# Performance work log

Hardware: AMD Instinct MI355X
Metric: run time of the kernel (lower is better)

The kernel has to match this reference:

```python
import jax, jax.numpy as jnp
from jax import lax
import numpy as np

D_MODEL = 512
D_PROJ = 256
PATCH = 4
NL = 8
D_STATE = 16
D_CONV = 4
EXPAND = 2
D_INNER = EXPAND * D_MODEL          # 1024
DT_RANK = (D_MODEL + 15) // 16      # 32
B = 4
SEQ = 1024
NF = 1
EPS = 1e-5


def setup_inputs() -> dict:
    key = jax.random.key(0)
    ks = jax.random.split(key, 12)
    s = 0.02
    def rn(k, shape):
        return jax.random.normal(k, shape, jnp.float32) * s
    A_init = jnp.log(jnp.arange(1, D_STATE + 1, dtype=jnp.float32))  # (n,)
    return {
        "time_series": jax.random.normal(ks[0], (B, SEQ, NF), jnp.float32),
        "mask": jnp.ones((B, SEQ), jnp.int32),
        "emb_w": rn(ks[1], (D_MODEL, PATCH)),
        "emb_b": jnp.zeros((D_MODEL,), jnp.float32),
        "norm_w": jnp.ones((NL, D_MODEL), jnp.float32),
        "in_w": rn(ks[2], (NL, 2, 2 * D_INNER, D_MODEL)),
        "conv_w": rn(ks[3], (NL, 2, D_INNER, D_CONV)),
        "conv_b": jnp.zeros((NL, 2, D_INNER), jnp.float32),
        "xproj_w": rn(ks[4], (NL, 2, DT_RANK + 2 * D_STATE, D_INNER)),
        "dt_w": rn(ks[5], (NL, 2, D_INNER, DT_RANK)),
        "dt_b": jnp.full((NL, 2, D_INNER), float(np.log(np.expm1(0.01))), jnp.float32),
        "A_log": jnp.broadcast_to(A_init, (NL, 2, D_INNER, D_STATE)) + jnp.zeros((NL, 2, D_INNER, D_STATE), jnp.float32),
        "Dp": jnp.ones((NL, 2, D_INNER), jnp.float32),
        "out_w": rn(ks[6], (NL, 2, D_MODEL, D_INNER)),
        "proj_w": rn(ks[7], (PATCH * D_PROJ, D_MODEL)),
        "proj_b": jnp.zeros((PATCH * D_PROJ,), jnp.float32),
    }


def rmsnorm(x, w):
    return x * lax.rsqrt(jnp.mean(x * x, axis=-1, keepdims=True) + EPS) * w


def mamba(x, in_w, conv_w, conv_b, xproj_w, dt_w, dt_b, A_log, Dp, out_w):
    # x: (B, L, D_MODEL)
    Bsz, L, _ = x.shape
    xz = jnp.einsum('bld,ed->ble', x, in_w)                 # (B,L,2*d_inner)
    u, z = jnp.split(xz, 2, axis=-1)                         # each (B,L,d_inner)
    # depthwise causal conv1d along L
    u_t = jnp.transpose(u, (0, 2, 1))                        # (B,d_inner,L)
    u_pad = jnp.pad(u_t, ((0, 0), (0, 0), (D_CONV - 1, 0)))
    conv = lax.conv_general_dilated(
        u_pad, conv_w[:, None, :], window_strides=(1,), padding='VALID',
        feature_group_count=D_INNER, dimension_numbers=('NCH', 'OIH', 'NCH'))
    u = jax.nn.silu(jnp.transpose(conv + conv_b[None, :, None], (0, 2, 1)))  # (B,L,d_inner)
    x_dbl = jnp.einsum('ble,re->blr', u, xproj_w)            # (B,L,dt_rank+2n)
    dt, Bm, C = jnp.split(x_dbl, [DT_RANK, DT_RANK + D_STATE], axis=-1)
    delta = jax.nn.softplus(jnp.einsum('blr,er->ble', dt, dt_w) + dt_b)  # (B,L,d_inner)
    A = -jnp.exp(A_log)                                      # (d_inner,n)

    def step(h, inp):
        d_t, B_t, C_t, u_t = inp                             # (B,e),(B,n),(B,n),(B,e)
        dA = jnp.exp(d_t[..., None] * A)                     # (B,e,n)
        h = dA * h + (d_t * u_t)[..., None] * B_t[:, None, :]
        y = jnp.einsum('ben,bn->be', h, C_t)
        return h, y

    h0 = jnp.zeros((Bsz, D_INNER, D_STATE), x.dtype)
    xs = (jnp.moveaxis(delta, 1, 0), jnp.moveaxis(Bm, 1, 0),
          jnp.moveaxis(C, 1, 0), jnp.moveaxis(u, 1, 0))
    _, ys = lax.scan(step, h0, xs)                           # ys: (L,B,e)
    y = jnp.moveaxis(ys, 0, 1) + u * Dp
    y = y * jax.nn.silu(z)
    return jnp.einsum('ble,de->bld', y, out_w)               # (B,L,D_MODEL)


def reference(time_series, mask, emb_w, emb_b, norm_w, in_w, conv_w, conv_b,
              xproj_w, dt_w, dt_b, A_log, Dp, out_w, proj_w, proj_b):
    Bsz, S, F_ = time_series.shape
    NP = S // PATCH  # S is a multiple of PATCH
    patches = time_series.reshape(Bsz, NP, PATCH, F_)
    patches = jnp.transpose(patches, (0, 3, 1, 2)).reshape(Bsz, F_ * NP, PATCH)
    x = patches @ emb_w.T + emb_b                            # (B, F*NP, D_MODEL)
    for i in range(NL):
        res = x
        xn = rmsnorm(x, norm_w[i])
        yf = mamba(xn, in_w[i, 0], conv_w[i, 0], conv_b[i, 0], xproj_w[i, 0],
                   dt_w[i, 0], dt_b[i, 0], A_log[i, 0], Dp[i, 0], out_w[i, 0])
        yb = mamba(jnp.flip(xn, axis=1), in_w[i, 1], conv_w[i, 1], conv_b[i, 1],
                   xproj_w[i, 1], dt_w[i, 1], dt_b[i, 1], A_log[i, 1], Dp[i, 1], out_w[i, 1])
        x = yf + jnp.flip(yb, axis=1) + res
    proj = x @ proj_w.T + proj_b                             # (B, F*NP, PATCH*D_PROJ)
    le = proj.reshape(Bsz, F_, NP, PATCH, D_PROJ)
    le = jnp.transpose(le, (0, 2, 3, 1, 4)).reshape(Bsz, NP * PATCH, F_, D_PROJ)
    return le[:, :S]
```

## Files before the change

### kernel.cpp

```cpp
#include <hip/hip_runtime.h>
#include <hip/hip_bf16.h>

#define DM 512
#define DI 1024
#define DSTATE 16
#define DTR 32
#define NLAYER 8
#define BS 4
#define LL 256
#define MT 1024
#define DPROJ 256
#define CL 32
#define NCH (LL/CL)

typedef unsigned short u16;
typedef unsigned int u32;
typedef __attribute__((ext_vector_type(8))) short short8;
typedef __attribute__((ext_vector_type(4))) float f32x4;

__device__ __forceinline__ float sigmoidf_(float x){ return 1.f/(1.f+__expf(-x)); }

__device__ __forceinline__ u16 f2bf(float f){
  unsigned u = __float_as_uint(f);
  u = (u + 0x7FFF + ((u>>16)&1)) >> 16;
  return (u16)u;
}
__device__ __forceinline__ float bf2f(u16 v){
  return __uint_as_float(((unsigned)v) << 16);
}

template<int CTRL>
__device__ __forceinline__ float dpp_ror_add(float x){
  int y = __builtin_amdgcn_update_dpp(0, __float_as_int(x), CTRL, 0xF, 0xF, false);
  return x + __int_as_float(y);
}
__device__ __forceinline__ float sum16_dpp(float x){
  x = dpp_ror_add<0x128>(x);
  x = dpp_ror_add<0x124>(x);
  x = dpp_ror_add<0x122>(x);
  x = dpp_ror_add<0x121>(x);
  return x;
}

__global__ __launch_bounds__(256) void embed_k(const float* __restrict__ ts,
    const float* __restrict__ ew, const float* __restrict__ eb, float* __restrict__ x){
  int idx = blockIdx.x*256 + threadIdx.x;
  int m = idx >> 9, d = idx & 511;
  int b = m >> 8, np_ = m & 255;
  const float* t0 = ts + b*1024 + np_*4;
  float acc = eb[d];
  #pragma unroll
  for (int p=0;p<4;p++) acc = fmaf(t0[p], ew[d*4+p], acc);
  x[idx] = acc;
}

#define WQUAR 1671168
__global__ __launch_bounds__(256) void wcastall_k(
    const float* __restrict__ w_in, const float* __restrict__ w_out,
    const float* __restrict__ w_xp, const float* __restrict__ w_pj,
    u16* __restrict__ dst){
  int t = blockIdx.x*256 + threadIdx.x;
  float4 v[4]; long e4s[4];
  #pragma unroll
  for (int ss=0; ss<4; ++ss){
    long e4 = ((long)t + (long)ss*WQUAR)*4;
    e4s[ss] = e4;
    const float* src; long o;
    if      (e4 < 16777216) { src = w_in;  o = e4; }
    else if (e4 < 25165824) { src = w_out; o = e4 - 16777216; }
    else if (e4 < 26214400) { src = w_xp;  o = e4 - 25165824; }
    else                    { src = w_pj;  o = e4 - 26214400; }
    v[ss] = *(const float4*)(src + o);
  }
  #pragma unroll
  for (int ss=0; ss<4; ++ss){
    ushort4 r; r.x=f2bf(v[ss].x); r.y=f2bf(v[ss].y); r.z=f2bf(v[ss].z); r.w=f2bf(v[ss].w);
    *(ushort4*)(dst + e4s[ss]) = r;
  }
}

__global__ __launch_bounds__(256) void rmscomb_k(float* __restrict__ x,
    const float* __restrict__ yout,
    const float* __restrict__ nw, u16* __restrict__ xnbf, u16* __restrict__ xnfbf){
  int m = blockIdx.x, t = threadIdx.x;
  int b = m>>8, l = m&255, mf = (b<<8)+(255-l);
  float2 v = *(const float2*)&x[(long)m*DM + t*2];
  if (yout){
    float2 f = *(const float2*)&yout[(long)m*DM + t*2];
    float2 g = *(const float2*)&yout[(long)MT*DM + (long)mf*DM + t*2];
    v.x += f.x + g.x; v.y += f.y + g.y;
    *(float2*)&x[(long)m*DM + t*2] = v;
  }
  float ss = v.x*v.x + v.y*v.y;
  ss += __shfl_down(ss,32); ss += __shfl_down(ss,16); ss += __shfl_down(ss,8);
  ss += __shfl_down(ss,4);  ss += __shfl_down(ss,2);  ss += __shfl_down(ss,1);
  __shared__ float ps[4];
  if ((t&63)==0) ps[t>>6] = ss;
  __syncthreads();
  float tot = ps[0]+ps[1]+ps[2]+ps[3];
  float rs = rsqrtf(tot*(1.f/DM) + 1e-5f);
  ushort2 o; o.x = f2bf(v.x*rs*nw[t*2]); o.y = f2bf(v.y*rs*nw[t*2+1]);
  *(ushort2*)&xnbf [(long)m *DM + t*2] = o;
  *(ushort2*)&xnfbf[(long)mf*DM + t*2] = o;
}

__global__ __launch_bounds__(256) void combcast_k(const float* __restrict__ x,
    const float* __restrict__ yout, u16* __restrict__ xbf){
  int idx = blockIdx.x*256 + threadIdx.x;
  int m = idx >> 7, c4 = idx & 127;
  int b = m>>8, l = m&255, mf = (b<<8)+(255-l);
  float4 r = ((const float4*)x)[idx];
  float4 f = ((const float4*)yout)[idx];
  float4 g = ((const float4*)(yout + (long)MT*DM))[(long)mf*128 + c4];
  ushort4 o;
  o.x = f2bf(r.x + f.x + g.x); o.y = f2bf(r.y + f.y + g.y);
  o.z = f2bf(r.z + f.z + g.z); o.w = f2bf(r.w + f.w + g.w);
  ((ushort4*)xbf)[idx] = o;
}

template<int BM,int BN,int SPLITK,int EPI>
__global__ __launch_bounds__(256) void mfma_nt(
    const u16* __restrict__ A, int lda, long sA,
    const u16* __restrict__ W, int ldw, long sW,
    const float* __restrict__ bias, u16* __restrict__ G,
    float* __restrict__ C, int ldc, long sC,
    int M, int N, int K)
{
  constexpr int WM = BM/2, WN = BN/2;
  constexpr int MI = WM/16, NI = WN/16;
  int z = blockIdx.z;
  int dir = z / SPLITK, kc = z % SPLITK;
  int Klen = K / SPLITK;
  int kbase = kc * Klen;
  A += (long)dir * sA;
  W += (long)dir * sW;
  if (SPLITK > 1) C += (long)z * M * N; else C += (long)dir * sC;
  if (EPI==4) G += (long)dir * (long)MT*DI;

  __shared__ u16 Al[BM*32];
  __shared__ u16 Wl[BN*32];
  int tid = threadIdx.x;
  int lane = tid & 63;
  int wave = tid >> 6;
  int wm0 = (wave>>1)*WM, wn0 = (wave&1)*WN;
  int m0 = blockIdx.y*BM, n0 = blockIdx.x*BN;
  int l16 = lane>>4, l15 = lane&15;

  f32x4 acc[MI][NI] = {};

  for (int k0=0; k0<Klen; k0+=32){
    #pragma unroll
    for (int it=0; it<BM*4/256; ++it){
      int ch = it*256 + tid;
      int row = ch % BM, kk = ch / BM;
      const u16* g = A + (long)(m0+row)*lda + kbase + k0 + kk*8;
      __builtin_amdgcn_global_load_lds(
          (const __attribute__((address_space(1))) void*)g,
          (__attribute__((address_space(3))) void*)(Al + ch*8), 16, 0, 0);
    }
    #pragma unroll
    for (int it=0; it<BN*4/256; ++it){
      int ch = it*256 + tid;
      int row = ch % BN, kk = ch / BN;
      const u16* g = W + (long)(n0+row)*ldw + kbase + k0 + kk*8;
      __builtin_amdgcn_global_load_lds(
          (const __attribute__((address_space(1))) void*)g,
          (__attribute__((address_space(3))) void*)(Wl + ch*8), 16, 0, 0);
    }
    __syncthreads();
    short8 a[MI], b[NI];
    #pragma unroll
    for (int i=0;i<MI;i++)
      a[i] = *(const short8*)&Al[(l16*BM + wm0 + i*16 + l15)*8];
    #pragma unroll
    for (int j=0;j<NI;j++)
      b[j] = *(const short8*)&Wl[(l16*BN + wn0 + j*16 + l15)*8];
    #pragma unroll
    for (int i=0;i<MI;i++)
      #pragma unroll
      for (int j=0;j<NI;j++)
        acc[i][j] = __builtin_amdgcn_mfma_f32_16x16x32_bf16(a[i], b[j], acc[i][j], 0,0,0);
    __syncthreads();
  }
  #pragma unroll
  for (int i=0;i<MI;i++){
    #pragma unroll
    for (int j=0;j<NI;j++){
      #pragma unroll
      for (int r=0;r<4;r++){
        int m = m0 + wm0 + i*16 + l16*4 + r;
        int n = n0 + wn0 + j*16 + l15;
        float v = acc[i][j][r];
        if (EPI==2){
          v += bias[n];
          int bb = m>>8, np_ = m&255, p = n>>8, dp = n&255;
          C[((long)(bb*1024 + np_*4 + p))*256 + dp] = v;
        } else if (EPI==4){
          if (n < 1024) C[(long)m*1024 + n] = v;
          else          G[(long)m*1024 + (n-1024)] = f2bf(v * sigmoidf_(v));
        } else {
          C[(long)m*ldc + n] = v;
        }
      }
    }
  }
}

__global__ __launch_bounds__(256) void xreduce_k(const float* __restrict__ part,
    float* __restrict__ xdbl){
  int idx = blockIdx.x*256 + threadIdx.x;
  int d = idx >> 16, off = idx & 65535;
  float s = 0.f;
  #pragma unroll
  for (int kc=0; kc<8; ++kc) s += part[((d*8+kc)<<16) + off];
  xdbl[idx] = s;
}

__global__ __launch_bounds__(256) void conv_silu_k(const float* __restrict__ xzu,
    const float* __restrict__ cw, const float* __restrict__ cb,
    u16* __restrict__ ubf){
  int idx = blockIdx.x*256 + threadIdx.x;
  int e = (idx & 255) * 4;
  int grp = idx >> 8;
  int dir = grp >> 8;
  int b   = (grp >> 6) & 3;
  int l0  = (grp & 63) * 4;
  long dm0 = (long)dir*MT + b*LL + l0;
  const float* w = cw + ((long)dir*DI + e)*4;
  float4 w0 = *(const float4*)&w[0];
  float4 w1 = *(const float4*)&w[4];
  float4 w2 = *(const float4*)&w[8];
  float4 w3 = *(const float4*)&w[12];
  float4 bias = *(const float4*)&cb[dir*DI + e];
  const float* src = xzu + dm0*DI + e;
  float4 vb[7];
  #pragma unroll
  for (int j=0;j<7;j++){
    int l = l0 - 3 + j;
    if (l >= 0) vb[j] = *(const float4*)&src[(long)(j-3)*DI];
    else        vb[j] = make_float4(0.f,0.f,0.f,0.f);
  }
  #pragma unroll
  for (int j=0;j<4;j++){
    float4 acc = bias;
    acc.x = fmaf(w0.x, vb[j].x,   acc.x); acc.x = fmaf(w0.y, vb[j+1].x, acc.x);
    acc.x = fmaf(w0.z, vb[j+2].x, acc.x); acc.x = fmaf(w0.w, vb[j+3].x, acc.x);
    acc.y = fmaf(w1.x, vb[j].y,   acc.y); acc.y = fmaf(w1.y, vb[j+1].y, acc.y);
    acc.y = fmaf(w1.z, vb[j+2].y, acc.y); acc.y = fmaf(w1.w, vb[j+3].y, acc.y);
    acc.z = fmaf(w2.x, vb[j].z,   acc.z); acc.z = fmaf(w2.y, vb[j+1].z, acc.z);
    acc.z = fmaf(w2.z, vb[j+2].z, acc.z); acc.z = fmaf(w2.w, vb[j+3].z, acc.z);
    acc.w = fmaf(w3.x, vb[j].w,   acc.w); acc.w = fmaf(w3.y, vb[j+1].w, acc.w);
    acc.w = fmaf(w3.z, vb[j+2].w, acc.w); acc.w = fmaf(w3.w, vb[j+3].w, acc.w);
    float vx = acc.x * sigmoidf_(acc.x);
    float vy = acc.y * sigmoidf_(acc.y);
    float vz = acc.z * sigmoidf_(acc.z);
    float vw = acc.w * sigmoidf_(acc.w);
    ushort4 o; o.x=f2bf(vx); o.y=f2bf(vy); o.z=f2bf(vz); o.w=f2bf(vw);
    *(ushort4*)&ubf[(dm0+j)*DI + e] = o;
  }
}

__global__ __launch_bounds__(256) void scan_k(
    const u16* __restrict__ ubf, const u16* __restrict__ gbf,
    const float* __restrict__ xdbl, const float* __restrict__ dtw,
    const float* __restrict__ dtb, const float* __restrict__ A_log,
    const float* __restrict__ Dp, u16* __restrict__ ygbf)
{
  int t = threadIdx.x;
  int n = t & 15, el = t >> 4;
  int id = blockIdx.x + 64*blockIdx.y + 256*blockIdx.z;
  int xcd = id & 7, slot = id >> 3;
  int ec = xcd*8 + (slot & 7);
  int bd = slot >> 3;
  int b = bd & 3, dir = bd >> 2;

  int e0 = ec*16, e = e0 + el;
  float Av = -__expf(A_log[((long)dir*DI + e)*16 + n]);
  float Dv = Dp[dir*DI + e];
  long mbase = (long)dir*MT + b*LL;
  const u16* up_ = ubf + mbase*DI;
  const u16* gp_ = gbf + mbase*DI;
  const float* xd_ = xdbl + mbase*64;
  u16* yp_ = ygbf + mbase*DI;

  float wrow[32];
  {
    const float* wr = dtw + ((long)dir*DI + e0 + n)*32;
    #pragma unroll
    for (int r4=0;r4<8;r4++) *(float4*)&wrow[r4*4] = *(const float4*)&wr[r4*4];
  }
  float dtbv = dtb[dir*DI + e0 + n];

  __shared__ float sDU[2][16][68];
  __shared__ float sBC[2][16][68];
  __shared__ float sdt[2][32][36];
  __shared__ float sy [32][20];

  float4 xv0, xv1; ushort4 uvv;
  auto load_pre = [&](int c){
    long l0 = (long)c*CL;
    int f0 = t, f1 = t + 256;
    xv0 = *(const float4*)&xd_[(l0 + (f0>>4))*64 + (f0&15)*4];
    xv1 = *(const float4*)&xd_[(l0 + (f1>>4))*64 + (f1&15)*4];
    if (t < 128) uvv = *(const ushort4*)&up_[(l0 + (t>>2))*DI + e0 + (t&3)*4];
  };
  auto write_pre = [&](int buf){
    #pragma unroll
    for (int h_=0; h_<2; ++h_){
      float4 xv = h_ ? xv1 : xv0;
      int f = t + h_*256;
      int row = f>>4, c4 = (f&15)*4;
      if (c4 < 32){
        *(float4*)&sdt[buf][row][c4] = xv;
      } else if (c4 < 48){
        int nb = c4 - 32;
        sBC[buf][nb  ][row*2] = xv.x; sBC[buf][nb+1][row*2] = xv.y;
        sBC[buf][nb+2][row*2] = xv.z; sBC[buf][nb+3][row*2] = xv.w;
      } else {
        int nb = c4 - 48;
        sBC[buf][nb  ][row*2+1] = xv.x; sBC[buf][nb+1][row*2+1] = xv.y;
        sBC[buf][nb+2][row*2+1] = xv.z; sBC[buf][nb+3][row*2+1] = xv.w;
      }
    }
    if (t < 128){
      int l = t>>2, e4 = (t&3)*4;
      sDU[buf][e4  ][l*2+1] = bf2f(uvv.x);
      sDU[buf][e4+1][l*2+1] = bf2f(uvv.y);
      sDU[buf][e4+2][l*2+1] = bf2f(uvv.z);
      sDU[buf][e4+3][l*2+1] = bf2f(uvv.w);
    }
  };

  load_pre(0);
  write_pre(0);
  load_pre(1);
  __syncthreads();

  float h = 0.f;
  int lp = t >> 4;
  for (int c = 0; c < NCH; ++c){
    int cur = c & 1;
    #pragma unroll
    for (int j=0;j<2;j++){
      int l = lp + j*16;
      float acc = dtbv;
      #pragma unroll
      for (int r4=0;r4<8;r4++){
        float4 d4 = *(const float4*)&sdt[cur][l][r4*4];
        acc = fmaf(d4.x, wrow[r4*4],   acc);
        acc = fmaf(d4.y, wrow[r4*4+1], acc);
        acc = fmaf(d4.z, wrow[r4*4+2], acc);
        acc = fmaf(d4.w, wrow[r4*4+3], acc);
      }
      acc = fmaxf(acc, 0.f) + __logf(1.f + __expf(-fabsf(acc)));
      sDU[cur][n][l*2] = acc;
    }
    ushort4 gv;
    if (t < 128) gv = *(const ushort4*)&gp_[((long)c*CL + (t>>2))*DI + e0 + (t&3)*4];
    __syncthreads();

    const float* pDU = &sDU[cur][el][0];
    const float* pBC = &sBC[cur][n][0];
    float4 duv[16], bcv[16];
    #pragma unroll
    for (int l2=0; l2<16; ++l2){
      duv[l2] = *(const float4*)&pDU[l2*4];
      bcv[l2] = *(const float4*)&pBC[l2*4];
    }
    float dA[32], sv[32], cv[32], ud[32];
    #pragma unroll
    for (int l2=0; l2<16; ++l2){
      dA[2*l2]   = __expf(duv[l2].x*Av);
      sv[2*l2]   = duv[l2].x*duv[l2].y*bcv[l2].x;
      cv[2*l2]   = bcv[l2].y;
      ud[2*l2]   = duv[l2].y*Dv;
      dA[2*l2+1] = __expf(duv[l2].z*Av);
      sv[2*l2+1] = duv[l2].z*duv[l2].w*bcv[l2].z;
      cv[2*l2+1] = bcv[l2].w;
      ud[2*l2+1] = duv[l2].w*Dv;
    }
    #pragma unroll
    for (int l=0; l<32; ++l){
      h = fmaf(dA[l], h, sv[l]);
      sv[l] = h;
    }
    #pragma unroll
    for (int l=0; l<32; ++l) sv[l] = sum16_dpp(sv[l]*cv[l]);
    if (n==0){
      #pragma unroll
      for (int l=0; l<32; ++l) sy[l][el] = sv[l] + ud[l];
    }
    __syncthreads();
    if (c+1 < NCH){
      write_pre(cur^1);
      if (c+2 < NCH) load_pre(c+2);
    }
    if (t < 128){
      float4 y4 = *(const float4*)&sy[t>>2][(t&3)*4];
      ushort4 o;
      o.x = f2bf(y4.x * bf2f(gv.x)); o.y = f2bf(y4.y * bf2f(gv.y));
      o.z = f2bf(y4.z * bf2f(gv.z)); o.w = f2bf(y4.w * bf2f(gv.w));
      *(ushort4*)&yp_[((long)c*CL + (t>>2))*DI + e0 + (t&3)*4] = o;
    }
    __syncthreads();
  }
}

extern "C" void kernel_launch(void* const* d_in, const int* in_sizes, int n_in,
                              void* d_out, int out_size, void* d_ws, size_t ws_size,
                              hipStream_t stream){
  const float* ts   = (const float*)d_in[0];
  const float* ew   = (const float*)d_in[2];
  const float* eb   = (const float*)d_in[3];
  const float* nw   = (const float*)d_in[4];
  const float* inw  = (const float*)d_in[5];
  const float* cw   = (const float*)d_in[6];
  const float* cb   = (const float*)d_in[7];
  const float* xpw  = (const float*)d_in[8];
  const float* dtw  = (const float*)d_in[9];
  const float* dtb  = (const float*)d_in[10];
  const float* alog = (const float*)d_in[11];
  const float* dpp  = (const float*)d_in[12];
  const float* outw = (const float*)d_in[13];
  const float* pw   = (const float*)d_in[14];
  const float* pb   = (const float*)d_in[15];
  float* out = (float*)d_out;

  float* ws   = (float*)d_ws;
  float* x    = ws;
  float* xzu  = ws + 524288;
  float* xdbl = ws + 2621440;
  float* yout = ws + 2752512;
  float* xpart= ws + 3801088;
  u16* ub     = (u16*)(ws + 4849664);
  u16* xn_bf  = ub;
  u16* u_bf   = ub + 1048576;
  u16* g_bf   = ub + 3145728;
  u16* yg_bf  = ub + 5242880;
  u16* x_bf   = ub + 7340032;
  u16* wb     = ub + 7864320;
  u16* wb_in  = wb;
  u16* wb_out = wb + 16777216;
  u16* wb_xp  = wb + 25165824;
  u16* wb_pj  = wb + 26214400;

  dim3 blk(256);

  embed_k<<<MT*DM/256, blk, 0, stream>>>(ts, ew, eb, x);
  wcastall_k<<<6528, blk, 0, stream>>>(inw, outw, xpw, pw, wb);

  for (int i=0;i<NLAYER;i++){
    rmscomb_k<<<MT, blk, 0, stream>>>(x, i ? yout : nullptr, nw + i*DM,
        xn_bf, xn_bf + MT*DM);
    mfma_nt<64,128,1,4><<<dim3(16,16,2), blk, 0, stream>>>(
        xn_bf, DM, (long)MT*DM, wb_in + (long)i*2097152, DM, 1048576,
        nullptr, g_bf, xzu, 1024, (long)MT*1024, MT, 2048, DM);
    conv_silu_k<<<512, blk, 0, stream>>>(xzu, cw + (long)i*2*DI*4, cb + i*2*DI, u_bf);
    mfma_nt<64,64,8,0><<<dim3(1,16,16), blk, 0, stream>>>(
        u_bf, DI, (long)MT*DI, wb_xp + (long)i*131072, DI, 65536,
        nullptr, nullptr, xpart, 64, 0, MT, 64, DI);
    xreduce_k<<<512, blk, 0, stream>>>(xpart, xdbl);
    scan_k<<<dim3(64, BS, 2), blk, 0, stream>>>(u_bf, g_bf, xdbl,
        dtw + (long)i*2*DI*DTR, dtb + (long)i*2*DI,
        alog + (long)i*2*DI*16, dpp + i*2*DI, yg_bf);
    mfma_nt<64,64,1,0><<<dim3(8,16,2), blk, 0, stream>>>(
        yg_bf, DI, (long)MT*DI, wb_out + (long)i*1048576, DI, 524288,
        nullptr, nullptr, yout, DM, (long)MT*DM, MT, DM, DI);
  }
  combcast_k<<<MT*DM/4/256, blk, 0, stream>>>(x, yout, x_bf);
  mfma_nt<64,64,1,2><<<dim3(16,16,1), blk, 0, stream>>>(
      x_bf, DM, 0, wb_pj, DM, 0, pb, nullptr, out, 1024, 0, MT, 1024, DM);
}
```

Baseline: 733.6 us.

## Fuse weight bf16 cast into GEMM loads and fold split-K reduce into scan

Removes the upfront kernel that converted all fp32 weights to bf16. Each GEMM now reads fp32 weights straight into registers, prefetching one K-step ahead, and converts them to bf16 before writing to LDS. It also drops the separate split-K reduction kernel: the scan kernel sums the eight partial x_proj results as it loads them. This saves two kernels and a large weight write and re-read, but doubles the weight bytes each GEMM block loads and adds conversion ALU work inside the GEMM loop.

```diff
diff --git a/kernel.cpp b/kernel.cpp
--- a/kernel.cpp
+++ b/kernel.cpp
@@ -52,31 +52,6 @@
   #pragma unroll
   for (int p=0;p<4;p++) acc = fmaf(t0[p], ew[d*4+p], acc);
   x[idx] = acc;
-}
-
-#define WQUAR 1671168
-__global__ __launch_bounds__(256) void wcastall_k(
-    const float* __restrict__ w_in, const float* __restrict__ w_out,
-    const float* __restrict__ w_xp, const float* __restrict__ w_pj,
-    u16* __restrict__ dst){
-  int t = blockIdx.x*256 + threadIdx.x;
-  float4 v[4]; long e4s[4];
-  #pragma unroll
-  for (int ss=0; ss<4; ++ss){
-    long e4 = ((long)t + (long)ss*WQUAR)*4;
-    e4s[ss] = e4;
-    const float* src; long o;
-    if      (e4 < 16777216) { src = w_in;  o = e4; }
-    else if (e4 < 25165824) { src = w_out; o = e4 - 16777216; }
-    else if (e4 < 26214400) { src = w_xp;  o = e4 - 25165824; }
-    else                    { src = w_pj;  o = e4 - 26214400; }
-    v[ss] = *(const float4*)(src + o);
-  }
-  #pragma unroll
-  for (int ss=0; ss<4; ++ss){
-    ushort4 r; r.x=f2bf(v[ss].x); r.y=f2bf(v[ss].y); r.z=f2bf(v[ss].z); r.w=f2bf(v[ss].w);
-    *(ushort4*)(dst + e4s[ss]) = r;
-  }
 }
 
 __global__ __launch_bounds__(256) void rmscomb_k(float* __restrict__ x,
@@ -121,13 +96,14 @@
 template<int BM,int BN,int SPLITK,int EPI>
 __global__ __launch_bounds__(256) void mfma_nt(
     const u16* __restrict__ A, int lda, long sA,
-    const u16* __restrict__ W, int ldw, long sW,
+    const float* __restrict__ W, int ldw, long sW,
     const float* __restrict__ bias, u16* __restrict__ G,
     float* __restrict__ C, int ldc, long sC,
     int M, int N, int K)
 {
   constexpr int WM = BM/2, WN = BN/2;
   constexpr int MI = WM/16, NI = WN/16;
+  constexpr int WCH = BN*4/256;
   int z = blockIdx.z;
   int dir = z / SPLITK, kc = z % SPLITK;
   int Klen = K / SPLITK;
@@ -146,7 +122,22 @@
   int m0 = blockIdx.y*BM, n0 = blockIdx.x*BN;
   int l16 = lane>>4, l15 = lane&15;
 
+  int wrow[WCH], wkk[WCH];
+  #pragma unroll
+  for (int it=0; it<WCH; ++it){
+    int ch = it*256 + tid;
+    wrow[it] = ch % BN; wkk[it] = ch / BN;
+  }
+
   f32x4 acc[MI][NI] = {};
+  float4 wreg[WCH][2];
+
+  #pragma unroll
+  for (int it=0; it<WCH; ++it){
+    const float* gw = W + (long)(n0+wrow[it])*ldw + kbase + wkk[it]*8;
+    wreg[it][0] = *(const float4*)gw;
+    wreg[it][1] = *(const float4*)(gw+4);
+  }
 
   for (int k0=0; k0<Klen; k0+=32){
     #pragma unroll
@@ -159,13 +150,22 @@
           (__attribute__((address_space(3))) void*)(Al + ch*8), 16, 0, 0);
     }
     #pragma unroll
-    for (int it=0; it<BN*4/256; ++it){
+    for (int it=0; it<WCH; ++it){
       int ch = it*256 + tid;
-      int row = ch % BN, kk = ch / BN;
-      const u16* g = W + (long)(n0+row)*ldw + kbase + k0 + kk*8;
-      __builtin_amdgcn_global_load_lds(
-          (const __attribute__((address_space(1))) void*)g,
-          (__attribute__((address_space(3))) void*)(Wl + ch*8), 16, 0, 0);
+      short8 pk;
+      pk[0]=(short)f2bf(wreg[it][0].x); pk[1]=(short)f2bf(wreg[it][0].y);
+      pk[2]=(short)f2bf(wreg[it][0].z); pk[3]=(short)f2bf(wreg[it][0].w);
+      pk[4]=(short)f2bf(wreg[it][1].x); pk[5]=(short)f2bf(wreg[it][1].y);
+      pk[6]=(short)f2bf(wreg[it][1].z); pk[7]=(short)f2bf(wreg[it][1].w);
+      *(short8*)&Wl[ch*8] = pk;
+    }
+    if (k0+32 < Klen){
+      #pragma unroll
+      for (int it=0; it<WCH; ++it){
+        const float* gw = W + (long)(n0+wrow[it])*ldw + kbase + k0+32 + wkk[it]*8;
+        wreg[it][0] = *(const float4*)gw;
+        wreg[it][1] = *(const float4*)(gw+4);
+      }
     }
     __syncthreads();
     short8 a[MI], b[NI];
@@ -204,16 +204,6 @@
       }
     }
   }
-}
-
-__global__ __launch_bounds__(256) void xreduce_k(const float* __restrict__ part,
-    float* __restrict__ xdbl){
-  int idx = blockIdx.x*256 + threadIdx.x;
-  int d = idx >> 16, off = idx & 65535;
-  float s = 0.f;
-  #pragma unroll
-  for (int kc=0; kc<8; ++kc) s += part[((d*8+kc)<<16) + off];
-  xdbl[idx] = s;
 }
 
 __global__ __launch_bounds__(256) void conv_silu_k(const float* __restrict__ xzu,
@@ -262,7 +252,7 @@
 
 __global__ __launch_bounds__(256) void scan_k(
     const u16* __restrict__ ubf, const u16* __restrict__ gbf,
-    const float* __restrict__ xdbl, const float* __restrict__ dtw,
+    const float* __restrict__ xpart, const float* __restrict__ dtw,
     const float* __restrict__ dtb, const float* __restrict__ A_log,
     const float* __restrict__ Dp, u16* __restrict__ ygbf)
 {
@@ -280,7 +270,8 @@
   long mbase = (long)dir*MT + b*LL;
   const u16* up_ = ubf + mbase*DI;
   const u16* gp_ = gbf + mbase*DI;
-  const float* xd_ = xdbl + mbase*64;
+  const float* xp_ = xpart + (((long)dir*8)<<16);
+  long mrow0 = (long)b*LL;
   u16* yp_ = ygbf + mbase*DI;
 
   float wrow[32];
@@ -300,8 +291,18 @@
   auto load_pre = [&](int c){
     long l0 = (long)c*CL;
     int f0 = t, f1 = t + 256;
-    xv0 = *(const float4*)&xd_[(l0 + (f0>>4))*64 + (f0&15)*4];
-    xv1 = *(const float4*)&xd_[(l0 + (f1>>4))*64 + (f1&15)*4];
+    long a0 = (mrow0 + l0 + (f0>>4))*64 + (f0&15)*4;
+    long a1 = (mrow0 + l0 + (f1>>4))*64 + (f1&15)*4;
+    float4 s0 = make_float4(0.f,0.f,0.f,0.f);
+    float4 s1 = make_float4(0.f,0.f,0.f,0.f);
+    #pragma unroll
+    for (int kc=0; kc<8; ++kc){
+      float4 p0 = *(const float4*)&xp_[((long)kc<<16) + a0];
+      float4 p1 = *(const float4*)&xp_[((long)kc<<16) + a1];
+      s0.x += p0.x; s0.y += p0.y; s0.z += p0.z; s0.w += p0.w;
+      s1.x += p1.x; s1.y += p1.y; s1.z += p1.z; s1.w += p1.w;
+    }
+    xv0 = s0; xv1 = s1;
     if (t < 128) uvv = *(const ushort4*)&up_[(l0 + (t>>2))*DI + e0 + (t&3)*4];
   };
   auto write_pre = [&](int buf){
@@ -429,45 +430,37 @@
   float* ws   = (float*)d_ws;
   float* x    = ws;
   float* xzu  = ws + 524288;
-  float* xdbl = ws + 2621440;
-  float* yout = ws + 2752512;
-  float* xpart= ws + 3801088;
-  u16* ub     = (u16*)(ws + 4849664);
+  float* yout = ws + 2621440;
+  float* xpart= ws + 3670016;
+  u16* ub     = (u16*)(ws + 4718592);
   u16* xn_bf  = ub;
   u16* u_bf   = ub + 1048576;
   u16* g_bf   = ub + 3145728;
   u16* yg_bf  = ub + 5242880;
   u16* x_bf   = ub + 7340032;
-  u16* wb     = ub + 7864320;
-  u16* wb_in  = wb;
-  u16* wb_out = wb + 16777216;
-  u16* wb_xp  = wb + 25165824;
-  u16* wb_pj  = wb + 26214400;
 
   dim3 blk(256);
 
   embed_k<<<MT*DM/256, blk, 0, stream>>>(ts, ew, eb, x);
-  wcastall_k<<<6528, blk, 0, stream>>>(inw, outw, xpw, pw, wb);
 
   for (int i=0;i<NLAYER;i++){
     rmscomb_k<<<MT, blk, 0, stream>>>(x, i ? yout : nullptr, nw + i*DM,
         xn_bf, xn_bf + MT*DM);
     mfma_nt<64,128,1,4><<<dim3(16,16,2), blk, 0, stream>>>(
-        xn_bf, DM, (long)MT*DM, wb_in + (long)i*2097152, DM, 1048576,
+        xn_bf, DM, (long)MT*DM, inw + (long)i*2*2048*DM, DM, (long)2048*DM,
         nullptr, g_bf, xzu, 1024, (long)MT*1024, MT, 2048, DM);
     conv_silu_k<<<512, blk, 0, stream>>>(xzu, cw + (long)i*2*DI*4, cb + i*2*DI, u_bf);
     mfma_nt<64,64,8,0><<<dim3(1,16,16), blk, 0, stream>>>(
-        u_bf, DI, (long)MT*DI, wb_xp + (long)i*131072, DI, 65536,
+        u_bf, DI, (long)MT*DI, xpw + (long)i*2*64*DI, DI, (long)64*DI,
         nullptr, nullptr, xpart, 64, 0, MT, 64, DI);
-    xreduce_k<<<512, blk, 0, stream>>>(xpart, xdbl);
-    scan_k<<<dim3(64, BS, 2), blk, 0, stream>>>(u_bf, g_bf, xdbl,
+    scan_k<<<dim3(64, BS, 2), blk, 0, stream>>>(u_bf, g_bf, xpart,
         dtw + (long)i*2*DI*DTR, dtb + (long)i*2*DI,
         alog + (long)i*2*DI*16, dpp + i*2*DI, yg_bf);
     mfma_nt<64,64,1,0><<<dim3(8,16,2), blk, 0, stream>>>(
-        yg_bf, DI, (long)MT*DI, wb_out + (long)i*1048576, DI, 524288,
+        yg_bf, DI, (long)MT*DI, outw + (long)i*2*DM*DI, DI, (long)DM*DI,
         nullptr, nullptr, yout, DM, (long)MT*DM, MT, DM, DI);
   }
   combcast_k<<<MT*DM/4/256, blk, 0, stream>>>(x, yout, x_bf);
   mfma_nt<64,64,1,2><<<dim3(16,16,1), blk, 0, stream>>>(
-      x_bf, DM, 0, wb_pj, DM, 0, pb, nullptr, out, 1024, 0, MT, 1024, DM);
-}
+      x_bf, DM, 0, pw, DM, 0, pb, nullptr, out, 1024, 0, MT, 1024, DM);
+}
```

Measured after the change: 841.6 us. +14.7%, slower.

## Read scan dt inputs directly from global memory and halve cast-kernel work per thread

Applied to the files above, without the earlier changes.

The scan kernel no longer stages the dt-rank part of xdbl in shared memory. Each thread now reads its 32-float dt row straight from global (cached) memory for the dt projection, which frees shared memory and removes half of the prefetch loads and stores. The weight-cast kernel now converts 2 chunks per thread instead of 4 and launches twice as many blocks. The trade-off is redundant global/L1 reads of the dt rows across threads, in exchange for lower LDS pressure and possibly higher occupancy.

```diff
diff --git a/kernel.cpp b/kernel.cpp
--- a/kernel.cpp
+++ b/kernel.cpp
@@ -54,28 +54,23 @@
   x[idx] = acc;
 }
 
-#define WQUAR 1671168
+#define WHALF 3342336
 __global__ __launch_bounds__(256) void wcastall_k(
     const float* __restrict__ w_in, const float* __restrict__ w_out,
     const float* __restrict__ w_xp, const float* __restrict__ w_pj,
     u16* __restrict__ dst){
   int t = blockIdx.x*256 + threadIdx.x;
-  float4 v[4]; long e4s[4];
-  #pragma unroll
-  for (int ss=0; ss<4; ++ss){
-    long e4 = ((long)t + (long)ss*WQUAR)*4;
-    e4s[ss] = e4;
+  #pragma unroll
+  for (int hh=0; hh<2; ++hh){
+    long e4 = ((long)t + (long)hh*WHALF)*4;
     const float* src; long o;
     if      (e4 < 16777216) { src = w_in;  o = e4; }
     else if (e4 < 25165824) { src = w_out; o = e4 - 16777216; }
     else if (e4 < 26214400) { src = w_xp;  o = e4 - 25165824; }
     else                    { src = w_pj;  o = e4 - 26214400; }
-    v[ss] = *(const float4*)(src + o);
-  }
-  #pragma unroll
-  for (int ss=0; ss<4; ++ss){
-    ushort4 r; r.x=f2bf(v[ss].x); r.y=f2bf(v[ss].y); r.z=f2bf(v[ss].z); r.w=f2bf(v[ss].w);
-    *(ushort4*)(dst + e4s[ss]) = r;
+    float4 v = *(const float4*)(src + o);
+    ushort4 r; r.x=f2bf(v.x); r.y=f2bf(v.y); r.z=f2bf(v.z); r.w=f2bf(v.w);
+    *(ushort4*)(dst + e4) = r;
   }
 }
 
@@ -293,34 +288,25 @@
 
   __shared__ float sDU[2][16][68];
   __shared__ float sBC[2][16][68];
-  __shared__ float sdt[2][32][36];
   __shared__ float sy [32][20];
 
-  float4 xv0, xv1; ushort4 uvv;
+  float4 xbc; ushort4 uvv;
   auto load_pre = [&](int c){
     long l0 = (long)c*CL;
-    int f0 = t, f1 = t + 256;
-    xv0 = *(const float4*)&xd_[(l0 + (f0>>4))*64 + (f0&15)*4];
-    xv1 = *(const float4*)&xd_[(l0 + (f1>>4))*64 + (f1&15)*4];
+    int row = t >> 3, c4 = (t & 7)*4;
+    xbc = *(const float4*)&xd_[(l0 + row)*64 + 32 + c4];
     if (t < 128) uvv = *(const ushort4*)&up_[(l0 + (t>>2))*DI + e0 + (t&3)*4];
   };
   auto write_pre = [&](int buf){
-    #pragma unroll
-    for (int h_=0; h_<2; ++h_){
-      float4 xv = h_ ? xv1 : xv0;
-      int f = t + h_*256;
-      int row = f>>4, c4 = (f&15)*4;
-      if (c4 < 32){
-        *(float4*)&sdt[buf][row][c4] = xv;
-      } else if (c4 < 48){
-        int nb = c4 - 32;
-        sBC[buf][nb  ][row*2] = xv.x; sBC[buf][nb+1][row*2] = xv.y;
-        sBC[buf][nb+2][row*2] = xv.z; sBC[buf][nb+3][row*2] = xv.w;
-      } else {
-        int nb = c4 - 48;
-        sBC[buf][nb  ][row*2+1] = xv.x; sBC[buf][nb+1][row*2+1] = xv.y;
-        sBC[buf][nb+2][row*2+1] = xv.z; sBC[buf][nb+3][row*2+1] = xv.w;
-      }
+    int row = t >> 3, c4 = (t & 7)*4;
+    if (c4 < 16){
+      int nb = c4;
+      sBC[buf][nb  ][row*2] = xbc.x; sBC[buf][nb+1][row*2] = xbc.y;
+      sBC[buf][nb+2][row*2] = xbc.z; sBC[buf][nb+3][row*2] = xbc.w;
+    } else {
+      int nb = c4 - 16;
+      sBC[buf][nb  ][row*2+1] = xbc.x; sBC[buf][nb+1][row*2+1] = xbc.y;
+      sBC[buf][nb+2][row*2+1] = xbc.z; sBC[buf][nb+3][row*2+1] = xbc.w;
     }
     if (t < 128){
       int l = t>>2, e4 = (t&3)*4;
@@ -343,10 +329,11 @@
     #pragma unroll
     for (int j=0;j<2;j++){
       int l = lp + j*16;
+      const float* row = &xd_[((long)c*CL + l)*64];
       float acc = dtbv;
       #pragma unroll
       for (int r4=0;r4<8;r4++){
-        float4 d4 = *(const float4*)&sdt[cur][l][r4*4];
+        float4 d4 = *(const float4*)&row[r4*4];
         acc = fmaf(d4.x, wrow[r4*4],   acc);
         acc = fmaf(d4.y, wrow[r4*4+1], acc);
         acc = fmaf(d4.z, wrow[r4*4+2], acc);
@@ -447,7 +434,7 @@
   dim3 blk(256);
 
   embed_k<<<MT*DM/256, blk, 0, stream>>>(ts, ew, eb, x);
-  wcastall_k<<<6528, blk, 0, stream>>>(inw, outw, xpw, pw, wb);
+  wcastall_k<<<13056, blk, 0, stream>>>(inw, outw, xpw, pw, wb);
 
   for (int i=0;i<NLAYER;i++){
     rmscomb_k<<<MT, blk, 0, stream>>>(x, i ? yout : nullptr, nw + i*DM,
```

Result: no change. 728.7 us (-0.7%).
